# Performance work log

Hardware: AMD Instinct MI355X
Metric: run time of the kernel (lower is better)

The kernel has to match this reference:

```python
import jax, jax.numpy as jnp
import numpy as np

HID_DIM = 512
N_HEADS = 8
HEAD_DIM = HID_DIM // N_HEADS  # 64
MAX_REL = 96
SEQ = 2048
BATCH = 4


def _rel_ids(length, max_rel=MAX_REL):
    # mirrors RelativePosition index construction (requires even length)
    rv = jnp.concatenate([jnp.arange(length // 2 + 1),
                          jnp.arange(length // 2 - 1, 0, -1)])
    dist = rv[None, :] - rv[:, None]              # [Lq, Lk]
    return jnp.clip(dist, -max_rel, max_rel) + max_rel


def setup_inputs() -> dict:
    key = jax.random.key(0)
    k1, k2, k3, k4, k5 = jax.random.split(key, 5)
    qkv = jax.random.normal(k1, (BATCH, SEQ, 3 * HID_DIM), dtype=jnp.float32)
    # xavier_uniform for [193, head_dim] tables
    lim = float(np.sqrt(6.0 / (2 * MAX_REL + 1 + HEAD_DIM)))
    rel_k_table = jax.random.uniform(k2, (2 * MAX_REL + 1, HEAD_DIM), jnp.float32, -lim, lim)
    rel_v_table = jax.random.uniform(k3, (2 * MAX_REL + 1, HEAD_DIM), jnp.float32, -lim, lim)
    lim_o = float(np.sqrt(1.0 / HID_DIM))
    Wo = jax.random.uniform(k4, (HID_DIM, HID_DIM), jnp.float32, -lim_o, lim_o)
    bo = jax.random.uniform(k5, (HID_DIM,), jnp.float32, -lim_o, lim_o)
    return {"qkv": qkv, "rel_k_table": rel_k_table, "rel_v_table": rel_v_table,
            "Wo": Wo, "bo": bo}


def reference(qkv, rel_k_table, rel_v_table, Wo, bo):
    B, S, W = qkv.shape
    H, dh = N_HEADS, HEAD_DIM
    q, k, v = jnp.split(qkv, 3, axis=2)           # each [B,S,D]

    qh = q.reshape(B, S, H, dh)                   # [B,S,H,dh]
    kh = k.reshape(B, S, H, dh)
    vh = v.reshape(B, S, H, dh)

    # content-content scores
    attn1 = jnp.einsum('bqhd,bkhd->bhqk', qh, kh)
    # content-position scores: gather relpos embeddings [Lq,Lk,dh]
    ids = _rel_ids(S)
    rk2 = rel_k_table[ids]                        # [S,S,dh]
    attn2 = jnp.einsum('bqhd,qkd->bhqk', qh, rk2)

    scale = jnp.sqrt(jnp.asarray(dh, jnp.float32))
    attn = jax.nn.softmax((attn1 + attn2) / scale, axis=-1)  # [B,H,S,S]

    # content-content values + content-position values
    w1 = jnp.einsum('bhqk,bkhd->bhqd', attn, vh)
    rv2 = rel_v_table[ids]                        # [S,S,dh]
    w2 = jnp.einsum('bhqk,qkd->bhqd', attn, rv2)

    x = (w1 + w2).transpose(0, 2, 1, 3).reshape(B, S, HID_DIM)
    return x @ Wo.T + bo
```

## Files before the change

### kernel.cpp

```cpp
#include <hip/hip_runtime.h>
#include <hip/hip_fp16.h>
#include <type_traits>


#define SEQ   2048
#define NHEAD 8
#define DH    64
#define HID   512
#define ROWW  1536
#define QT    64
#define GPS   196

#define C_L2E8 0.180336880111120f

typedef _Float16 h16;
typedef __attribute__((ext_vector_type(4))) float    f32x4;
typedef __attribute__((ext_vector_type(8))) _Float16 h16x8;
typedef __attribute__((ext_vector_type(4))) _Float16 h16x4;

static __device__ __forceinline__ h16x8 pack8(float4 a, float4 b) {
  h16x8 r;
  r[0]=(h16)a.x; r[1]=(h16)a.y; r[2]=(h16)a.z; r[3]=(h16)a.w;
  r[4]=(h16)b.x; r[5]=(h16)b.y; r[6]=(h16)b.z; r[7]=(h16)b.w;
  return r;
}

struct alignas(16) SmBase {
  h16 attnRh[64][224];
  h16 K[64][64];
  h16 Vt[64][64];
  h16 P[4][16][64];
};
struct alignas(16) SmFull {
  h16 attnRh[64][224];
  h16 K[64][64];
  h16 Vt[64][64];
  h16 P[4][16][64];
  h16 projh[64][194];
};

__global__ __launch_bounds__(256)
void proj_gemm(const float* __restrict__ qkv, const float* __restrict__ relk,
               h16* __restrict__ gproj)
{
  const int qt = blockIdx.x, h = blockIdx.y, b = blockIdx.z;
  const int tid = (int)threadIdx.x;
  const int w = tid >> 6, l = tid & 63, l15 = l & 15, l4 = l >> 4;
  const int q0 = qt * 64;

  const float* qr = qkv + ((size_t)(b*SEQ) + q0 + w*16 + l15) * ROWW + h*DH + l4*8;
  h16x8 aq0 = pack8(*(const float4*)(qr),      *(const float4*)(qr + 4));
  h16x8 aq1 = pack8(*(const float4*)(qr + 32), *(const float4*)(qr + 36));

  h16* orow = gproj + ((size_t)(b*NHEAD + h)*SEQ + q0 + w*16) * GPS;

#pragma unroll
  for (int nt = 0; nt < 13; ++nt) {
    const int n0 = nt * 16;
    const int rc = (n0 + l15 > 192) ? 192 : n0 + l15;
    const float* rkp = relk + rc*DH + l4*8;
    h16x8 b0 = pack8(*(const float4*)(rkp),      *(const float4*)(rkp + 4));
    h16x8 b1 = pack8(*(const float4*)(rkp + 32), *(const float4*)(rkp + 36));
    f32x4 z = {};
    z = __builtin_amdgcn_mfma_f32_16x16x32_f16(aq0, b0, z, 0, 0, 0);
    z = __builtin_amdgcn_mfma_f32_16x16x32_f16(aq1, b1, z, 0, 0, 0);
    if (n0 + l15 < GPS) {
#pragma unroll
      for (int j = 0; j < 4; ++j)
        orow[(size_t)(l4*4 + j)*GPS + n0 + l15] = (h16)z[j];
    }
  }
}

__global__ __launch_bounds__(256)
void wo_convert(const float* __restrict__ Wo, h16* __restrict__ Woh)
{
  const size_t i = (size_t)blockIdx.x * 256 + threadIdx.x;
  float4 v = *(const float4*)(Wo + i*4);
  h16x4 o; o[0]=(h16)v.x; o[1]=(h16)v.y; o[2]=(h16)v.z; o[3]=(h16)v.w;
  *(h16x4*)(Woh + i*4) = o;
}

__global__ void relv_pack(const float* __restrict__ relv, h16* __restrict__ relvh)
{
  const int bi = (int)blockIdx.x;
  const int l = (int)threadIdx.x, l15 = l & 15, l4 = l >> 4;
  const int kblk = bi >> 2, vc = bi & 3;
  h16x8 o;
#pragma unroll
  for (int e = 0; e < 8; ++e) {
    const int k = kblk*32 + l4*8 + e;
    o[e] = (k < 193) ? (h16)relv[k*DH + vc*16 + l15] : (h16)0.f;
  }
  *(h16x8*)(relvh + ((size_t)bi*64 + l)*8) = o;
}

template<bool GP>
__global__ __launch_bounds__(256, 3)
void attn_fused(const float* __restrict__ qkv,
                const float* __restrict__ relk,
                const float* __restrict__ relv,
                const h16* __restrict__ gproj,
                const h16* __restrict__ relvh,
                h16* __restrict__ xout)
{
  using SM = typename std::conditional<GP, SmBase, SmFull>::type;
  __shared__ SM sm;

  const int wg = (int)blockIdx.x;
  const int id = (wg & 7) * 128 + (wg >> 3);
  const int qt = id & 31, h = (id >> 5) & 7, b = id >> 8;

  const int tid = (int)threadIdx.x;
  const int w = tid >> 6, l = tid & 63, l15 = l & 15, l4 = l >> 4;
  const int q0 = qt * QT;
  const int dl = l, kq = w;

  const float* qbase = qkv + ((size_t)(b*SEQ) + q0) * ROWW + h*DH;
  const float* kbase = qkv + (size_t)(b*SEQ) * ROWW + HID   + h*DH;
  const float* vbase = qkv + (size_t)(b*SEQ) * ROWW + 2*HID + h*DH;
  const h16* gprow = gproj + ((size_t)(b*NHEAD + h)*SEQ + q0 + w*16) * GPS;

  {
    int4* az = (int4*)&sm.attnRh[0][0];
#pragma unroll 2
    for (int i = tid; i < (int)(sizeof(sm.attnRh)/16); i += 256)
      az[i] = make_int4(0,0,0,0);
  }

  if constexpr (!GP) {
    const int prow = tid >> 2, psub = tid & 3;
    const float* qrow = qbase + (size_t)prow * ROWW;
    float4 qv[16];
#pragma unroll
    for (int c = 0; c < 16; ++c) qv[c] = *(const float4*)(qrow + c*4);
    for (int r = psub; r < 193; r += 4) {
      const float4* rk = (const float4*)(relk + r*DH);
      float acc1 = 0.f;
#pragma unroll
      for (int c = 0; c < 16; ++c) {
        float4 tt = rk[c];
        acc1 += qv[c].x*tt.x + qv[c].y*tt.y + qv[c].z*tt.z + qv[c].w*tt.w;
      }
      sm.projh[prow][r] = (h16)acc1;
    }
  }

  h16x8 aq0, aq1;
  {
    const float* qr = qbase + (size_t)(w*16 + l15) * ROWW + l4*8;
    aq0 = pack8(*(const float4*)(qr),      *(const float4*)(qr + 4));
    aq1 = pack8(*(const float4*)(qr + 32), *(const float4*)(qr + 36));
  }

  int rvq[4];
#pragma unroll
  for (int j = 0; j < 4; ++j) {
    int qg = q0 + w*16 + l4*4 + j;
    rvq[j] = (qg <= 1024) ? qg : (2048 - qg);
  }

  const int qa = q0 + w*16, qb = qa + 15;
  const int rqa = (qa <= 1024) ? qa : 2048 - qa;
  const int rqb = (qb <= 1024) ? qb : 2048 - qb;
  const int rvqmin = rqa < rqb ? rqa : rqb;
  const int rvqmax = (qa <= 1024 && 1024 <= qb) ? 1024 : (rqa > rqb ? rqa : rqb);

  auto classify = [&](int KT) -> int {
    const int ka = KT*64, kb = ka + 63;
    const int ra = (ka <= 1024) ? ka : 2048 - ka;
    const int rb = (kb <= 1024) ? kb : 2048 - kb;
    const int rmin = ra < rb ? ra : rb;
    const int rmax = (ka <= 1024 && 1024 <= kb) ? 1024 : (ra > rb ? ra : rb);
    if (rmax <= rvqmin - 96) return 0;
    if (rmin >= rvqmax + 96) return 2;
    return 1;
  };

  f32x4 acc[4] = {};
  float lsum[4] = {0.f,0.f,0.f,0.f};
  float c0[4]   = {0.f,0.f,0.f,0.f};
  float c192[4] = {0.f,0.f,0.f,0.f};

  float4 kreg[4];
  float  vreg[4][4];

  auto kvIssue = [&](int KT) {
    const int kk = KT * 64;
#pragma unroll
    for (int m = 0; m < 4; ++m) {
      const int idx4 = tid + 256*m;
      kreg[m] = *(const float4*)(kbase + (size_t)(kk + (idx4>>4))*ROWW + (idx4&15)*4);
    }
#pragma unroll
    for (int m = 0; m < 4; ++m)
#pragma unroll
      for (int e = 0; e < 4; ++e)
        vreg[m][e] = vbase[(size_t)(kk + m*16 + kq*4 + e)*ROWW + dl];
  };

  auto kvWrite = [&]() {
#pragma unroll
    for (int m = 0; m < 4; ++m) {
      const int idx4 = tid + 256*m;
      const int kr = idx4 >> 4, c4 = idx4 & 15;
      h16x4 t; t[0]=(h16)kreg[m].x; t[1]=(h16)kreg[m].y; t[2]=(h16)kreg[m].z; t[3]=(h16)kreg[m].w;
      *(h16x4*)(&sm.K[kr][(c4*4) ^ ((kr & 7) << 3)]) = t;
    }
#pragma unroll
    for (int m = 0; m < 4; ++m) {
      h16x4 u; u[0]=(h16)vreg[m][0]; u[1]=(h16)vreg[m][1]; u[2]=(h16)vreg[m][2]; u[3]=(h16)vreg[m][3];
      *(h16x4*)(&sm.Vt[dl][(m*16 + kq*4) ^ ((dl & 7) << 3)]) = u;
    }
  };

  int cls = classify(0);
  kvIssue(0);
  kvWrite();
  __syncthreads();

  float proj0f[4], proj192f[4], C0e[4], C192e[4];
  if constexpr (GP) {
#pragma unroll
    for (int j = 0; j < 4; ++j) {
      proj0f[j]   = (float)gprow[(size_t)(l4*4 + j)*GPS + 0];
      proj192f[j] = (float)gprow[(size_t)(l4*4 + j)*GPS + 192];
    }
  } else {
#pragma unroll
    for (int j = 0; j < 4; ++j) {
      proj0f[j]   = (float)sm.projh[w*16 + l4*4 + j][0];
      proj192f[j] = (float)sm.projh[w*16 + l4*4 + j][192];
    }
  }
#pragma unroll
  for (int j = 0; j < 4; ++j) {
    C0e[j]   = exp2f(proj0f[j]   * C_L2E8);
    C192e[j] = exp2f(proj192f[j] * C_L2E8);
  }

  const int kswz = (l15 & 7) << 3;

  for (int kt = 0; kt < 32; ++kt) {
    const int kk = kt * 64;

    f32x4 sc[4];
#pragma unroll
    for (int ct = 0; ct < 4; ++ct) {
      h16x8 kb0 = *(const h16x8*)(&sm.K[ct*16 + l15][(l4*8) ^ kswz]);
      h16x8 kb1 = *(const h16x8*)(&sm.K[ct*16 + l15][(32 + l4*8) ^ kswz]);
      f32x4 z = {};
      z = __builtin_amdgcn_mfma_f32_16x16x32_f16(aq0, kb0, z, 0, 0, 0);
      z = __builtin_amdgcn_mfma_f32_16x16x32_f16(aq1, kb1, z, 0, 0, 0);
      sc[ct] = z;
    }

    if (kt < 31) kvIssue(kt + 1);

    if (cls == 1) {
#pragma unroll
      for (int ct = 0; ct < 4; ++ct) {
        const int kg = kk + ct*16 + l15;
        const int rvk = (kg <= 1024) ? kg : (2048 - kg);
#pragma unroll
        for (int j = 0; j < 4; ++j) {
          const int rowL = w*16 + l4*4 + j;
          int dd = rvk - rvq[j];
          dd = dd < -96 ? -96 : (dd > 96 ? 96 : dd);
          const int bin = dd + 96;
          float pj;
          if constexpr (GP) {
            pj = (bin == 0) ? proj0f[j]
               : (bin == 192) ? proj192f[j]
               : (float)gprow[(size_t)(l4*4 + j)*GPS + bin];
          } else {
            pj = (float)sm.projh[rowL][bin];
          }
          const float p = exp2f((sc[ct][j] + pj) * C_L2E8);
          lsum[j] += p;
          if (bin == 0)        c0[j]   += p;
          else if (bin == 192) c192[j] += p;
          else {
            h16 old = sm.attnRh[rowL][bin];
            sm.attnRh[rowL][bin] = old + (h16)p;
          }
          sm.P[w][l4*4 + j][(ct*16 + l15) ^ (((l4*4 + j) & 7) << 3)] = (h16)p;
        }
      }
    } else if (cls == 0) {
#pragma unroll
      for (int ct = 0; ct < 4; ++ct) {
#pragma unroll
        for (int j = 0; j < 4; ++j) {
          const float p = exp2f(sc[ct][j] * C_L2E8) * C0e[j];
          lsum[j] += p;
          c0[j]   += p;
          sm.P[w][l4*4 + j][(ct*16 + l15) ^ (((l4*4 + j) & 7) << 3)] = (h16)p;
        }
      }
    } else {
#pragma unroll
      for (int ct = 0; ct < 4; ++ct) {
#pragma unroll
        for (int j = 0; j < 4; ++j) {
          const float p = exp2f(sc[ct][j] * C_L2E8) * C192e[j];
          lsum[j] += p;
          c192[j] += p;
          sm.P[w][l4*4 + j][(ct*16 + l15) ^ (((l4*4 + j) & 7) << 3)] = (h16)p;
        }
      }
    }

    {
      h16x8 pa0 = *(const h16x8*)(&sm.P[w][l15][(l4*8) ^ kswz]);
      h16x8 pa1 = *(const h16x8*)(&sm.P[w][l15][(32 + l4*8) ^ kswz]);
#pragma unroll
      for (int vc = 0; vc < 4; ++vc) {
        const int d = vc*16 + l15;
        h16x8 vb0 = *(const h16x8*)(&sm.Vt[d][(l4*8) ^ kswz]);
        h16x8 vb1 = *(const h16x8*)(&sm.Vt[d][(32 + l4*8) ^ kswz]);
        acc[vc] = __builtin_amdgcn_mfma_f32_16x16x32_f16(pa0, vb0, acc[vc], 0, 0, 0);
        acc[vc] = __builtin_amdgcn_mfma_f32_16x16x32_f16(pa1, vb1, acc[vc], 0, 0, 0);
      }
    }

    __syncthreads();
    if (kt < 31) { kvWrite(); cls = classify(kt + 1); }
    __syncthreads();
  }

#pragma unroll
  for (int j = 0; j < 4; ++j) {
    for (int mask = 1; mask < 16; mask <<= 1) {
      c0[j]   += __shfl_xor(c0[j],   mask);
      c192[j] += __shfl_xor(c192[j], mask);
      lsum[j] += __shfl_xor(lsum[j], mask);
    }
  }
  if (l15 == 0) {
#pragma unroll
    for (int j = 0; j < 4; ++j) {
      sm.attnRh[w*16 + l4*4 + j][0]   = (h16)c0[j];
      sm.attnRh[w*16 + l4*4 + j][192] = (h16)c192[j];
    }
  }

#pragma unroll
  for (int kb6 = 0; kb6 < 7; ++kb6) {
    h16x8 pa = *(const h16x8*)(&sm.attnRh[w*16 + l15][kb6*32 + l4*8]);
#pragma unroll
    for (int vc = 0; vc < 4; ++vc) {
      h16x8 bf = *(const h16x8*)(relvh + ((size_t)((kb6*4 + vc)*64 + l))*8);
      acc[vc] = __builtin_amdgcn_mfma_f32_16x16x32_f16(pa, bf, acc[vc], 0, 0, 0);
    }
  }

  float inv[4];
#pragma unroll
  for (int j = 0; j < 4; ++j) inv[j] = 1.f / lsum[j];
#pragma unroll
  for (int vc = 0; vc < 4; ++vc) {
#pragma unroll
    for (int j = 0; j < 4; ++j) {
      const int row16 = l4*4 + j;
      const int col   = vc*16 + l15;
      xout[((size_t)(b*SEQ) + q0 + w*16 + row16) * HID + h*DH + col] =
          (h16)(acc[vc][j] * inv[j]);
    }
  }
}

template<bool WH>
__global__ __launch_bounds__(256)
void out_proj(const h16* __restrict__ xh,
              const float* __restrict__ Wo,
              const h16* __restrict__ Woh,
              const float* __restrict__ bo,
              float* __restrict__ out)
{
  const int tid = (int)threadIdx.x;
  const int w = tid >> 6, l = tid & 63, l15 = l & 15, l4 = l >> 4;
  const int m0 = blockIdx.x * 64 + w * 16;
  const int n0 = blockIdx.y * 64;
  f32x4 acc[4] = {};
  const h16* arow = xh + (size_t)(m0 + l15) * HID + l4*8;
#pragma unroll
  for (int ks = 0; ks < 16; ++ks) {
    h16x8 a = *(const h16x8*)(arow + ks*32);
#pragma unroll
    for (int ct = 0; ct < 4; ++ct) {
      h16x8 bfrag;
      if constexpr (WH) {
        bfrag = *(const h16x8*)(Woh + (size_t)(n0 + ct*16 + l15) * HID + ks*32 + l4*8);
      } else {
        const float* wrow = Wo + (size_t)(n0 + ct*16 + l15) * HID + ks*32 + l4*8;
        bfrag = pack8(*(const float4*)wrow, *(const float4*)(wrow + 4));
      }
      acc[ct] = __builtin_amdgcn_mfma_f32_16x16x32_f16(a, bfrag, acc[ct], 0, 0, 0);
    }
  }
#pragma unroll
  for (int ct = 0; ct < 4; ++ct) {
    const int col = n0 + ct*16 + l15;
    const float bv = bo[col];
#pragma unroll
    for (int j = 0; j < 4; ++j)
      out[(size_t)(m0 + l4*4 + j) * HID + col] = acc[ct][j] + bv;
  }
}

extern "C" void kernel_launch(void* const* d_in, const int* in_sizes, int n_in,
                              void* d_out, int out_size, void* d_ws, size_t ws_size,
                              hipStream_t stream)
{
  const float* qkv  = (const float*)d_in[0];
  const float* relk = (const float*)d_in[1];
  const float* relv = (const float*)d_in[2];
  const float* Wo   = (const float*)d_in[3];
  const float* bo   = (const float*)d_in[4];
  float* out = (float*)d_out;

  const size_t sz_xh    = (size_t)4*SEQ*HID*2;
  const size_t sz_gproj = (size_t)4*NHEAD*SEQ*GPS*2;
  const size_t sz_woh   = (size_t)HID*HID*2;
  const size_t sz_relvh = (size_t)28*64*8*2;

  h16* xh = (h16*)d_ws;

  const size_t off_gproj = sz_xh;
  const size_t off_woh   = off_gproj + sz_gproj;
  const size_t off_relvh = off_woh + sz_woh;
  const size_t need      = off_relvh + sz_relvh;

  if (ws_size >= need) {
    h16* gproj  = (h16*)((char*)d_ws + off_gproj);
    h16* woh    = (h16*)((char*)d_ws + off_woh);
    h16* relvh  = (h16*)((char*)d_ws + off_relvh);
    relv_pack<<<dim3(28), 64, 0, stream>>>(relv, relvh);
    proj_gemm<<<dim3(SEQ/64, NHEAD, 4), 256, 0, stream>>>(qkv, relk, gproj);
    wo_convert<<<dim3(HID*HID/4/256), 256, 0, stream>>>(Wo, woh);
    attn_fused<true><<<dim3(1024), 256, 0, stream>>>(qkv, relk, relv, gproj, relvh, xh);
    out_proj<true><<<dim3((4*SEQ)/64, HID/64), 256, 0, stream>>>(xh, Wo, woh, bo, out);
  } else {
    h16* relvh = (h16*)((char*)d_ws + sz_xh);
    relv_pack<<<dim3(28), 64, 0, stream>>>(relv, relvh);
    attn_fused<false><<<dim3(1024), 256, 0, stream>>>(qkv, relk, relv, nullptr, relvh, xh);
    out_proj<false><<<dim3((4*SEQ)/64, HID/64), 256, 0, stream>>>(xh, Wo, nullptr, bo, out);
  }
}
```

Before: 373.6 us.

## Double-buffer K/V tiles in LDS and prefetch relpos gathers one tile ahead

K and V^T shared tiles become double-buffered, so each step writes the next tile while computing the current one and loads global data two tiles ahead. This replaces two barriers per iteration with one. The relative-position bin computation and projection gather for the next tile are issued early to hide their latency. The softmax sum for the boundary bins is folded in once at the end, and the precomputed exp constants are dropped in favour of adding the projection before exp2. In exchange, LDS use grows and launch bounds drop from 3 to 2 blocks per SM, lowering occupancy and raising register pressure.

```diff
diff --git a/kernel.cpp b/kernel.cpp
--- a/kernel.cpp
+++ b/kernel.cpp
@@ -27,14 +27,14 @@
 
 struct alignas(16) SmBase {
   h16 attnRh[64][224];
-  h16 K[64][64];
-  h16 Vt[64][64];
+  h16 K[2][64][64];
+  h16 Vt[2][64][64];
   h16 P[4][16][64];
 };
 struct alignas(16) SmFull {
   h16 attnRh[64][224];
-  h16 K[64][64];
-  h16 Vt[64][64];
+  h16 K[2][64][64];
+  h16 Vt[2][64][64];
   h16 P[4][16][64];
   h16 projh[64][194];
 };
@@ -96,7 +96,7 @@
 }
 
 template<bool GP>
-__global__ __launch_bounds__(256, 3)
+__global__ __launch_bounds__(256, 2)
 void attn_fused(const float* __restrict__ qkv,
                 const float* __restrict__ relk,
                 const float* __restrict__ relv,
@@ -184,6 +184,8 @@
 
   float4 kreg[4];
   float  vreg[4][4];
+  int    bins[4][4];
+  float  pvf[4][4];
 
   auto kvIssue = [&](int KT) {
     const int kk = KT * 64;
@@ -199,27 +201,50 @@
         vreg[m][e] = vbase[(size_t)(kk + m*16 + kq*4 + e)*ROWW + dl];
   };
 
-  auto kvWrite = [&]() {
+  auto kvWrite = [&](int buf) {
 #pragma unroll
     for (int m = 0; m < 4; ++m) {
       const int idx4 = tid + 256*m;
       const int kr = idx4 >> 4, c4 = idx4 & 15;
       h16x4 t; t[0]=(h16)kreg[m].x; t[1]=(h16)kreg[m].y; t[2]=(h16)kreg[m].z; t[3]=(h16)kreg[m].w;
-      *(h16x4*)(&sm.K[kr][(c4*4) ^ ((kr & 7) << 3)]) = t;
+      *(h16x4*)(&sm.K[buf][kr][(c4*4) ^ ((kr & 7) << 3)]) = t;
     }
 #pragma unroll
     for (int m = 0; m < 4; ++m) {
       h16x4 u; u[0]=(h16)vreg[m][0]; u[1]=(h16)vreg[m][1]; u[2]=(h16)vreg[m][2]; u[3]=(h16)vreg[m][3];
-      *(h16x4*)(&sm.Vt[dl][(m*16 + kq*4) ^ ((dl & 7) << 3)]) = u;
+      *(h16x4*)(&sm.Vt[buf][dl][(m*16 + kq*4) ^ ((dl & 7) << 3)]) = u;
+    }
+  };
+
+  float proj0f[4], proj192f[4];
+
+  auto gatherIssue = [&](int KT) {
+#pragma unroll
+    for (int ct = 0; ct < 4; ++ct) {
+      const int kg = KT*64 + ct*16 + l15;
+      const int rvk = (kg <= 1024) ? kg : (2048 - kg);
+#pragma unroll
+      for (int j = 0; j < 4; ++j) {
+        int dd = rvk - rvq[j];
+        dd = dd < -96 ? -96 : (dd > 96 ? 96 : dd);
+        const int bin = dd + 96;
+        bins[ct][j] = bin;
+        if constexpr (GP) {
+          if (bin > 0 && bin < 192)
+            pvf[ct][j] = (float)gprow[(size_t)(l4*4 + j)*GPS + bin];
+          else
+            pvf[ct][j] = (bin == 0) ? proj0f[j] : proj192f[j];
+        }
+      }
     }
   };
 
   int cls = classify(0);
   kvIssue(0);
-  kvWrite();
+  kvWrite(0);
+  kvIssue(1);
   __syncthreads();
 
-  float proj0f[4], proj192f[4], C0e[4], C192e[4];
   if constexpr (GP) {
 #pragma unroll
     for (int j = 0; j < 4; ++j) {
@@ -233,54 +258,44 @@
       proj192f[j] = (float)sm.projh[w*16 + l4*4 + j][192];
     }
   }
-#pragma unroll
-  for (int j = 0; j < 4; ++j) {
-    C0e[j]   = exp2f(proj0f[j]   * C_L2E8);
-    C192e[j] = exp2f(proj192f[j] * C_L2E8);
-  }
+  if (cls == 1) gatherIssue(0);
 
   const int kswz = (l15 & 7) << 3;
 
   for (int kt = 0; kt < 32; ++kt) {
-    const int kk = kt * 64;
+    const int cur = kt & 1;
 
     f32x4 sc[4];
 #pragma unroll
     for (int ct = 0; ct < 4; ++ct) {
-      h16x8 kb0 = *(const h16x8*)(&sm.K[ct*16 + l15][(l4*8) ^ kswz]);
-      h16x8 kb1 = *(const h16x8*)(&sm.K[ct*16 + l15][(32 + l4*8) ^ kswz]);
+      h16x8 kb0 = *(const h16x8*)(&sm.K[cur][ct*16 + l15][(l4*8) ^ kswz]);
+      h16x8 kb1 = *(const h16x8*)(&sm.K[cur][ct*16 + l15][(32 + l4*8) ^ kswz]);
       f32x4 z = {};
       z = __builtin_amdgcn_mfma_f32_16x16x32_f16(aq0, kb0, z, 0, 0, 0);
       z = __builtin_amdgcn_mfma_f32_16x16x32_f16(aq1, kb1, z, 0, 0, 0);
       sc[ct] = z;
     }
 
-    if (kt < 31) kvIssue(kt + 1);
+    if (kt < 31) kvWrite(cur ^ 1);
+    if (kt < 30) kvIssue(kt + 2);
 
     if (cls == 1) {
 #pragma unroll
       for (int ct = 0; ct < 4; ++ct) {
-        const int kg = kk + ct*16 + l15;
-        const int rvk = (kg <= 1024) ? kg : (2048 - kg);
 #pragma unroll
         for (int j = 0; j < 4; ++j) {
           const int rowL = w*16 + l4*4 + j;
-          int dd = rvk - rvq[j];
-          dd = dd < -96 ? -96 : (dd > 96 ? 96 : dd);
-          const int bin = dd + 96;
+          const int bin = bins[ct][j];
           float pj;
-          if constexpr (GP) {
-            pj = (bin == 0) ? proj0f[j]
-               : (bin == 192) ? proj192f[j]
-               : (float)gprow[(size_t)(l4*4 + j)*GPS + bin];
-          } else {
+          if constexpr (GP) pj = pvf[ct][j];
+          else {
             pj = (float)sm.projh[rowL][bin];
           }
           const float p = exp2f((sc[ct][j] + pj) * C_L2E8);
-          lsum[j] += p;
           if (bin == 0)        c0[j]   += p;
           else if (bin == 192) c192[j] += p;
           else {
+            lsum[j] += p;
             h16 old = sm.attnRh[rowL][bin];
             sm.attnRh[rowL][bin] = old + (h16)p;
           }
@@ -292,9 +307,8 @@
       for (int ct = 0; ct < 4; ++ct) {
 #pragma unroll
         for (int j = 0; j < 4; ++j) {
-          const float p = exp2f(sc[ct][j] * C_L2E8) * C0e[j];
-          lsum[j] += p;
-          c0[j]   += p;
+          const float p = exp2f((sc[ct][j] + proj0f[j]) * C_L2E8);
+          c0[j] += p;
           sm.P[w][l4*4 + j][(ct*16 + l15) ^ (((l4*4 + j) & 7) << 3)] = (h16)p;
         }
       }
@@ -303,30 +317,31 @@
       for (int ct = 0; ct < 4; ++ct) {
 #pragma unroll
         for (int j = 0; j < 4; ++j) {
-          const float p = exp2f(sc[ct][j] * C_L2E8) * C192e[j];
-          lsum[j] += p;
+          const float p = exp2f((sc[ct][j] + proj192f[j]) * C_L2E8);
           c192[j] += p;
           sm.P[w][l4*4 + j][(ct*16 + l15) ^ (((l4*4 + j) & 7) << 3)] = (h16)p;
         }
       }
     }
 
+    const int clsN = (kt < 31) ? classify(kt + 1) : 0;
+    if (kt < 31 && clsN == 1) gatherIssue(kt + 1);
+
     {
       h16x8 pa0 = *(const h16x8*)(&sm.P[w][l15][(l4*8) ^ kswz]);
       h16x8 pa1 = *(const h16x8*)(&sm.P[w][l15][(32 + l4*8) ^ kswz]);
 #pragma unroll
       for (int vc = 0; vc < 4; ++vc) {
         const int d = vc*16 + l15;
-        h16x8 vb0 = *(const h16x8*)(&sm.Vt[d][(l4*8) ^ kswz]);
-        h16x8 vb1 = *(const h16x8*)(&sm.Vt[d][(32 + l4*8) ^ kswz]);
+        h16x8 vb0 = *(const h16x8*)(&sm.Vt[cur][d][(l4*8) ^ kswz]);
+        h16x8 vb1 = *(const h16x8*)(&sm.Vt[cur][d][(32 + l4*8) ^ kswz]);
         acc[vc] = __builtin_amdgcn_mfma_f32_16x16x32_f16(pa0, vb0, acc[vc], 0, 0, 0);
         acc[vc] = __builtin_amdgcn_mfma_f32_16x16x32_f16(pa1, vb1, acc[vc], 0, 0, 0);
       }
     }
 
-    __syncthreads();
-    if (kt < 31) { kvWrite(); cls = classify(kt + 1); }
-    __syncthreads();
+    cls = clsN;
+    if (kt < 31) __syncthreads();
   }
 
 #pragma unroll
@@ -336,6 +351,7 @@
       c192[j] += __shfl_xor(c192[j], mask);
       lsum[j] += __shfl_xor(lsum[j], mask);
     }
+    lsum[j] += c0[j] + c192[j];
   }
   if (l15 == 0) {
 #pragma unroll
```

Result: faster. 351.0 us (-6.1%).
